# Kernel tuning notes

Measured on AMD Instinct MI355X. Metric: run time of the kernel, lower is better.

The kernel has to match this reference:

```python
import jax, jax.numpy as jnp
import numpy as np

B, N, D, H = 4, 1024, 1024, 16
DH = D // H
MLP = 4 * D
EPS = 1e-6


def setup_inputs() -> dict:
    key = jax.random.key(0)
    ks = jax.random.split(key, 16)
    s = lambda fan_in: 1.0 / np.sqrt(fan_in)
    inp = {
        "x": jax.random.normal(ks[0], (B, N, D), jnp.float32),
        "c": jax.random.normal(ks[1], (B, D), jnp.float32),
        # weights stored (in, out); torch Linear is x @ W.T + b
        "Wq": jax.random.normal(ks[2], (D, D), jnp.float32) * s(D),
        "bq": jnp.zeros((D,), jnp.float32),
        "Wkv": jax.random.normal(ks[3], (D, 2 * D), jnp.float32) * s(D),
        "bkv": jnp.zeros((2 * D,), jnp.float32),
        "Wo": jax.random.normal(ks[4], (D, D), jnp.float32) * s(D),
        "bo": jnp.zeros((D,), jnp.float32),
        "W1": jax.random.normal(ks[5], (D, MLP), jnp.float32) * s(D),
        "b1": jnp.zeros((MLP,), jnp.float32),
        "W2": jax.random.normal(ks[6], (MLP, D), jnp.float32) * s(MLP),
        "b2": jnp.zeros((D,), jnp.float32),
        "Wada": jax.random.normal(ks[7], (D, 6 * D), jnp.float32) * s(D),
        "bada": jnp.zeros((6 * D,), jnp.float32),
    }
    return inp


def _layernorm(h):
    mu = jnp.mean(h, axis=-1, keepdims=True)
    var = jnp.mean(jnp.square(h - mu), axis=-1, keepdims=True)
    return (h - mu) / jnp.sqrt(var + EPS)


def _modulate(h, shift, scale):
    return h * (1.0 + scale[:, None, :]) + shift[:, None, :]


def reference(x, c, Wq, bq, Wkv, bkv, Wo, bo, W1, b1, W2, b2, Wada, bada):
    scale = DH ** -0.5
    mod = jax.nn.silu(c) @ Wada + bada  # [B, 6D]
    sh_msa, sc_msa, g_msa, sh_mlp, sc_mlp, g_mlp = jnp.split(mod, 6, axis=-1)

    # --- attention branch ---
    h = _modulate(_layernorm(x), sh_msa, sc_msa)
    q = (h @ Wq + bq).reshape(B, N, H, DH)
    kv = h @ Wkv + bkv
    k, v = jnp.split(kv, 2, axis=-1)
    k = k.reshape(B, N, H, DH)
    v = v.reshape(B, N, H, DH)
    sim = jnp.einsum("bihd,bjhd->bhij", q, k) * scale  # [B,H,N,N]
    attn = jax.nn.softmax(sim, axis=-1)
    out = jnp.einsum("bhij,bjhd->bihd", attn, v).reshape(B, N, D)
    out = out @ Wo + bo
    x = x + g_msa[:, None, :] * out

    # --- MLP branch ---
    h2 = _modulate(_layernorm(x), sh_mlp, sc_mlp)
    m = jax.nn.gelu(h2 @ W1 + b1, approximate=True) @ W2 + b2
    x = x + g_mlp[:, None, :] * m
    return x
```

## Files before the change

kernel.cpp:

```cpp
#include <hip/hip_runtime.h>
#include <hip/hip_bf16.h>
#include <cstdint>

typedef __attribute__((ext_vector_type(4))) float f32x4;
typedef __attribute__((ext_vector_type(16))) float f32x16;
typedef __attribute__((ext_vector_type(8))) short s16x8;
typedef __attribute__((ext_vector_type(4))) unsigned u32x4;
typedef unsigned short u16;

#define B_  4
#define N_  1024
#define D_  1024
#define H_  16
#define DH_ 64
#define M_  4096
#define SIXD 6144

#define WAITV(n) asm volatile("s_waitcnt vmcnt(" #n ")" ::: "memory")

__device__ __forceinline__ u16 f2bf(float f) {
    unsigned u = __builtin_bit_cast(unsigned, f);
    unsigned r = (u + 0x7fffu + ((u >> 16) & 1u)) >> 16;
    return (u16)r;
}

__device__ __forceinline__ unsigned cvtpk(float a, float b) {
    unsigned r;
    asm("v_cvt_pk_bf16_f32 %0, %1, %2" : "=v"(r) : "v"(a), "v"(b));
    return r;
}

__device__ __forceinline__ void gload16(const void* g, void* l) {
    __builtin_amdgcn_global_load_lds((const __attribute__((address_space(1))) void*)g,
                                     (__attribute__((address_space(3))) void*)l,
                                     16, 0, 0);
}

__global__ __launch_bounds__(256) void prep_all(const float* __restrict__ Wq,
                                                const float* __restrict__ Wkv,
                                                const float* __restrict__ Wo,
                                                const float* __restrict__ W1,
                                                const float* __restrict__ W2,
                                                const float* __restrict__ c,
                                                const float* __restrict__ Wada,
                                                u16* __restrict__ wqkvT,
                                                u16* __restrict__ woT,
                                                u16* __restrict__ w1T,
                                                u16* __restrict__ w2T,
                                                float* __restrict__ modp) {
    int id = blockIdx.x;
    int tid = threadIdx.x;
    if (id < 768) {
        __shared__ float sc[128];
        int colblk = id % 24, b = (id / 24) & 3, ks = id / 96;
        int col = colblk * 256 + tid;
        int k0 = ks * 128;
        if (tid < 128) {
            float v = c[b * D_ + k0 + tid];
            sc[tid] = v / (1.f + __expf(-v));
        }
        __syncthreads();
        float a0 = 0.f, a1 = 0.f, a2 = 0.f, a3 = 0.f;
#pragma unroll 4
        for (int k = 0; k < 128; k += 4) {
            a0 = fmaf(sc[k + 0], Wada[(size_t)(k0 + k + 0) * SIXD + col], a0);
            a1 = fmaf(sc[k + 1], Wada[(size_t)(k0 + k + 1) * SIXD + col], a1);
            a2 = fmaf(sc[k + 2], Wada[(size_t)(k0 + k + 2) * SIXD + col], a2);
            a3 = fmaf(sc[k + 3], Wada[(size_t)(k0 + k + 3) * SIXD + col], a3);
        }
        modp[(size_t)(ks * 4 + b) * SIXD + col] = (a0 + a1) + (a2 + a3);
        return;
    }
    int t_ = id - 768;
    const float* in; u16* outp; int R, C, loc;
    if (t_ < 256)       { in = Wq;  outp = wqkvT;           R = 1024; C = 1024; loc = t_; }
    else if (t_ < 768)  { in = Wkv; outp = wqkvT + 1048576; R = 1024; C = 2048; loc = t_ - 256; }
    else if (t_ < 1024) { in = Wo;  outp = woT;             R = 1024; C = 1024; loc = t_ - 768; }
    else if (t_ < 2048) { in = W1;  outp = w1T;             R = 1024; C = 4096; loc = t_ - 1024; }
    else                { in = W2;  outp = w2T;             R = 4096; C = 1024; loc = t_ - 2048; }
    int tpc = C >> 6;
    int bx = loc % tpc, by = loc / tpc;
    __shared__ float t[64][65];
    int r0 = by * 64, c0 = bx * 64;
    int l16 = tid & 15, grp = tid >> 4;
#pragma unroll
    for (int i = 0; i < 4; ++i) {
        int rr = grp + 16 * i;
        float4 v = *(const float4*)(in + (size_t)(r0 + rr) * C + c0 + l16 * 4);
        t[rr][l16 * 4 + 0] = v.x;
        t[rr][l16 * 4 + 1] = v.y;
        t[rr][l16 * 4 + 2] = v.z;
        t[rr][l16 * 4 + 3] = v.w;
    }
    __syncthreads();
#pragma unroll
    for (int i = 0; i < 4; ++i) {
        int cc = grp + 16 * i;
        ushort4 o;
        o.x = f2bf(t[l16 * 4 + 0][cc]);
        o.y = f2bf(t[l16 * 4 + 1][cc]);
        o.z = f2bf(t[l16 * 4 + 2][cc]);
        o.w = f2bf(t[l16 * 4 + 3][cc]);
        *(ushort4*)(outp + (size_t)(c0 + cc) * R + r0 + l16 * 4) = o;
    }
}

__global__ __launch_bounds__(256) void reduce_mod(const float* __restrict__ modp,
                                                  const float* __restrict__ bada,
                                                  float* __restrict__ mod) {
    int col = blockIdx.x * 256 + threadIdx.x;
    int b = blockIdx.y;
    float s = bada[col];
#pragma unroll
    for (int ks = 0; ks < 8; ++ks)
        s += modp[(size_t)(ks * 4 + b) * SIXD + col];
    mod[b * SIXD + col] = s;
}

__global__ __launch_bounds__(256) void ln_mod(const float* __restrict__ x,
                                              const float* __restrict__ mod,
                                              int shift_c, int scale_c,
                                              u16* __restrict__ h) {
    int row = blockIdx.x;
    int b = row >> 10;
    int tid = threadIdx.x, w = tid >> 6;
    float4 xv = ((const float4*)(x + (size_t)row * D_))[tid];
    float s  = xv.x + xv.y + xv.z + xv.w;
    float s2 = xv.x * xv.x + xv.y * xv.y + xv.z * xv.z + xv.w * xv.w;
#pragma unroll
    for (int m = 1; m <= 32; m <<= 1) { s += __shfl_xor(s, m); s2 += __shfl_xor(s2, m); }
    __shared__ float red[8];
    if ((tid & 63) == 0) { red[w * 2] = s; red[w * 2 + 1] = s2; }
    __syncthreads();
    float S  = red[0] + red[2] + red[4] + red[6];
    float S2 = red[1] + red[3] + red[5] + red[7];
    float mu = S * (1.f / D_);
    float var = S2 * (1.f / D_) - mu * mu;
    float rstd = rsqrtf(var + 1e-6f);
    int d0 = tid * 4;
    float4 shv = *(const float4*)(mod + b * SIXD + shift_c * D_ + d0);
    float4 scv = *(const float4*)(mod + b * SIXD + scale_c * D_ + d0);
    ushort4 o;
    o.x = f2bf((xv.x - mu) * rstd * (1.f + scv.x) + shv.x);
    o.y = f2bf((xv.y - mu) * rstd * (1.f + scv.y) + shv.y);
    o.z = f2bf((xv.z - mu) * rstd * (1.f + scv.z) + shv.z);
    o.w = f2bf((xv.w - mu) * rstd * (1.f + scv.w) + shv.w);
    *(ushort4*)(h + (size_t)row * D_ + d0) = o;
}

__global__ __launch_bounds__(512) void gemm_qkv(const u16* __restrict__ A,
                                                const u16* __restrict__ Bt,
                                                const float* __restrict__ bias,
                                                const float* __restrict__ bias2,
                                                u16* __restrict__ out,
                                                int M, int Nn, int K) {
    __shared__ char lds[2][32768];
    const int tid = threadIdx.x;
    const int w = tid >> 6, lane = tid & 63;
    const int li = lane & 15, lg = lane >> 4;
    const int nwg = gridDim.x * gridDim.y;
    const int flat = blockIdx.y * gridDim.x + blockIdx.x;
    const int wg = (flat & 7) * (nwg >> 3) + (flat >> 3);
    const int m0 = (wg / gridDim.x) * 128, n0 = (wg % gridDim.x) * 128;
    const int wr = w >> 1, wc = w & 1;

    f32x4 acc[2][4];
#pragma unroll
    for (int i = 0; i < 2; ++i)
#pragma unroll
        for (int j = 0; j < 4; ++j) acc[i][j] = (f32x4){0.f, 0.f, 0.f, 0.f};

    auto STAGE = [&](int kk, char* buf) {
#pragma unroll
        for (int j = 0; j < 4; ++j) {
            int basec = j * 512 + w * 64;
            int idx = basec + lane;
            int idl = idx & 1023;
            int row = idl >> 3, cc = idl & 7;
            const u16* src;
            if (idx < 1024)
                src = A + (size_t)(m0 + row) * K + kk + ((cc ^ (row & 7)) << 3);
            else
                src = Bt + (size_t)(n0 + row) * K + kk + ((cc ^ (row & 7)) << 3);
            gload16(src, buf + basec * 16);
        }
    };

    const int nt = K >> 6;
    STAGE(0, lds[0]);
    __syncthreads();
    int cur = 0;
    for (int t = 0; t < nt; ++t) {
        if (t + 1 < nt) { STAGE((t + 1) << 6, lds[cur ^ 1]); WAITV(4); }
        else WAITV(0);
        __builtin_amdgcn_s_barrier();
        __builtin_amdgcn_sched_barrier(0);
        const char* Ab = lds[cur];
        const char* Bb = lds[cur] + 16384;
#pragma unroll
        for (int hh = 0; hh < 2; ++hh) {
            s16x8 af[2], bfr[4];
#pragma unroll
            for (int mi = 0; mi < 2; ++mi) {
                int r = wr * 32 + mi * 16 + li;
                af[mi] = *(const s16x8*)(Ab + r * 128 + (((hh * 4 + lg) ^ (r & 7)) << 4));
            }
#pragma unroll
            for (int nj = 0; nj < 4; ++nj) {
                int r = wc * 64 + nj * 16 + li;
                bfr[nj] = *(const s16x8*)(Bb + r * 128 + (((hh * 4 + lg) ^ (r & 7)) << 4));
            }
#pragma unroll
            for (int mi = 0; mi < 2; ++mi)
#pragma unroll
                for (int nj = 0; nj < 4; ++nj)
                    acc[mi][nj] = __builtin_amdgcn_mfma_f32_16x16x32_bf16(
                        af[mi], bfr[nj], acc[mi][nj], 0, 0, 0);
        }
        __builtin_amdgcn_s_barrier();
        cur ^= 1;
    }

#pragma unroll
    for (int mi = 0; mi < 2; ++mi) {
#pragma unroll
        for (int nj = 0; nj < 4; ++nj) {
            int col = n0 + wc * 64 + nj * 16 + li;
            float bv = (col < D_) ? bias[col] : bias2[col - D_];
#pragma unroll
            for (int rg = 0; rg < 4; ++rg) {
                int grow = m0 + wr * 32 + mi * 16 + 4 * lg + rg;
                float v = acc[mi][nj][rg] + bv;
                int b = grow >> 10, n = grow & 1023;
                if (col < D_) {
                    int hd = col >> 6, dh = col & 63;
                    out[(((size_t)(b * H_ + hd)) * N_ + n) * DH_ + dh] = f2bf(v);
                } else if (col < 2 * D_) {
                    int c2 = col - D_;
                    int hd = c2 >> 6, dh = c2 & 63;
                    out[4194304u + (((size_t)(b * H_ + hd)) * N_ + n) * DH_ + dh] = f2bf(v);
                } else {
                    int c2 = col - 2 * D_;
                    int hd = c2 >> 6, dh = c2 & 63;
                    out[8388608u + (((size_t)(b * H_ + hd)) * DH_ + dh) * N_ + n] = f2bf(v);
                }
            }
        }
    }
}

template <int EPI>
__global__ __launch_bounds__(512) void gemm_bt(const u16* __restrict__ A,
                                               const u16* __restrict__ Bt,
                                               const float* __restrict__ bias,
                                               void* __restrict__ out,
                                               const float* __restrict__ xres,
                                               const float* __restrict__ mod,
                                               int M, int Nn, int K, int gate_c) {
    __shared__ char lds[2][32768];
    const int tid = threadIdx.x;
    const int w = tid >> 6, lane = tid & 63;
    const int li = lane & 15, lg = lane >> 4;
    const int nwg = gridDim.x * gridDim.y;
    const int flat = blockIdx.y * gridDim.x + blockIdx.x;
    const int wg = (flat & 7) * (nwg >> 3) + (flat >> 3);
    const int m0 = (wg / gridDim.x) * 128, n0 = (wg % gridDim.x) * 128;
    const int wr = w >> 1, wc = w & 1;

    f32x4 acc[2][4];
#pragma unroll
    for (int i = 0; i < 2; ++i)
#pragma unroll
        for (int j = 0; j < 4; ++j) acc[i][j] = (f32x4){0.f, 0.f, 0.f, 0.f};

    auto STAGE = [&](int kk, char* buf) {
#pragma unroll
        for (int j = 0; j < 4; ++j) {
            int basec = j * 512 + w * 64;
            int idx = basec + lane;
            int idl = idx & 1023;
            int row = idl >> 3, cc = idl & 7;
            const u16* src;
            if (idx < 1024)
                src = A + (size_t)(m0 + row) * K + kk + ((cc ^ (row & 7)) << 3);
            else
                src = Bt + (size_t)(n0 + row) * K + kk + ((cc ^ (row & 7)) << 3);
            gload16(src, buf + basec * 16);
        }
    };

    const int nt = K >> 6;
    STAGE(0, lds[0]);
    __syncthreads();
    int cur = 0;
    for (int t = 0; t < nt; ++t) {
        if (t + 1 < nt) { STAGE((t + 1) << 6, lds[cur ^ 1]); WAITV(4); }
        else WAITV(0);
        __builtin_amdgcn_s_barrier();
        __builtin_amdgcn_sched_barrier(0);
        const char* Ab = lds[cur];
        const char* Bb = lds[cur] + 16384;
#pragma unroll
        for (int hh = 0; hh < 2; ++hh) {
            s16x8 af[2], bfr[4];
#pragma unroll
            for (int mi = 0; mi < 2; ++mi) {
                int r = wr * 32 + mi * 16 + li;
                af[mi] = *(const s16x8*)(Ab + r * 128 + (((hh * 4 + lg) ^ (r & 7)) << 4));
            }
#pragma unroll
            for (int nj = 0; nj < 4; ++nj) {
                int r = wc * 64 + nj * 16 + li;
                bfr[nj] = *(const s16x8*)(Bb + r * 128 + (((hh * 4 + lg) ^ (r & 7)) << 4));
            }
#pragma unroll
            for (int mi = 0; mi < 2; ++mi)
#pragma unroll
                for (int nj = 0; nj < 4; ++nj)
                    acc[mi][nj] = __builtin_amdgcn_mfma_f32_16x16x32_bf16(
                        af[mi], bfr[nj], acc[mi][nj], 0, 0, 0);
        }
        __builtin_amdgcn_s_barrier();
        cur ^= 1;
    }

#pragma unroll
    for (int mi = 0; mi < 2; ++mi) {
#pragma unroll
        for (int nj = 0; nj < 4; ++nj) {
            int col = n0 + wc * 64 + nj * 16 + li;
            float bv = bias[col];
#pragma unroll
            for (int rg = 0; rg < 4; ++rg) {
                int grow = m0 + wr * 32 + mi * 16 + 4 * lg + rg;
                float v = acc[mi][nj][rg] + bv;
                int b = grow >> 10;
                size_t off = (size_t)grow * D_ + col;
                float g = mod[b * SIXD + gate_c * D_ + col];
                ((float*)out)[off] = xres[off] + g * v;
            }
        }
    }
}

__global__ __launch_bounds__(512, 2) void gemm256_gelu(const u16* __restrict__ A,
                                                       const u16* __restrict__ Bt,
                                                       const float* __restrict__ bias,
                                                       u16* __restrict__ out,
                                                       int M, int Nn, int K) {
    __shared__ char lds[2][65536];
    const int tid = threadIdx.x;
    const int w = tid >> 6, lane = tid & 63;
    const int li = lane & 15, lg = lane >> 4;
    const int wr = w >> 1, wc = w & 1;

    const int flat = blockIdx.x;
    const int wg = (flat & 7) * 32 + (flat >> 3);
    const int mg = wg >> 6, r_ = wg & 63;
    const int mt = mg * 4 + (r_ & 3), nt_ = r_ >> 2;
    const int m0 = mt * 256, n0 = nt_ * 256;

    f32x4 acc[4][8];
#pragma unroll
    for (int i = 0; i < 4; ++i)
#pragma unroll
        for (int j = 0; j < 8; ++j) acc[i][j] = (f32x4){0.f, 0.f, 0.f, 0.f};

    auto STAGE = [&](int kk, char* buf) {
#pragma unroll
        for (int j = 0; j < 4; ++j) {
            int basec = j * 512 + w * 64;
            int idx = basec + lane;
            int row = idx >> 3, cc = idx & 7;
            gload16(A + (size_t)(m0 + row) * K + kk + ((cc ^ (row & 7)) << 3),
                    buf + basec * 16);
            gload16(Bt + (size_t)(n0 + row) * K + kk + ((cc ^ (row & 7)) << 3),
                    buf + 32768 + basec * 16);
        }
    };

    const int nt = K >> 6;
    STAGE(0, lds[0]);
    __syncthreads();
    int cur = 0;
    for (int t = 0; t < nt; ++t) {
        if (t + 1 < nt) STAGE((t + 1) << 6, lds[cur ^ 1]);
        const char* Ab = lds[cur];
        const char* Bb = lds[cur] + 32768;
#pragma unroll
        for (int hh = 0; hh < 2; ++hh) {
            s16x8 af[4], bfr[8];
#pragma unroll
            for (int mi = 0; mi < 4; ++mi) {
                int r = wr * 64 + mi * 16 + li;
                af[mi] = *(const s16x8*)(Ab + r * 128 + (((hh * 4 + lg) ^ (r & 7)) << 4));
            }
#pragma unroll
            for (int nj = 0; nj < 8; ++nj) {
                int r = wc * 128 + nj * 16 + li;
                bfr[nj] = *(const s16x8*)(Bb + r * 128 + (((hh * 4 + lg) ^ (r & 7)) << 4));
            }
#pragma unroll
            for (int mi = 0; mi < 4; ++mi)
#pragma unroll
                for (int nj = 0; nj < 8; ++nj)
                    acc[mi][nj] = __builtin_amdgcn_mfma_f32_16x16x32_bf16(
                        af[mi], bfr[nj], acc[mi][nj], 0, 0, 0);
        }
        __syncthreads();
        cur ^= 1;
    }

#pragma unroll
    for (int nj = 0; nj < 8; ++nj) {
        int col = n0 + wc * 128 + nj * 16 + li;
        float bv = bias[col];
#pragma unroll
        for (int mi = 0; mi < 4; ++mi) {
#pragma unroll
            for (int rg = 0; rg < 4; ++rg) {
                int grow = m0 + wr * 64 + mi * 16 + 4 * lg + rg;
                float v = acc[mi][nj][rg] + bv;
                float u = 0.7978845608028654f * v * (1.f + 0.044715f * v * v);
                u = fminf(fmaxf(u, -15.f), 15.f);
                float e = __expf(2.f * u);
                float th = (e - 1.f) / (e + 1.f);
                out[(size_t)grow * (size_t)Nn + col] = f2bf(0.5f * v * (1.f + th));
            }
        }
    }
}

__global__ __launch_bounds__(256) void attn2(const u16* __restrict__ q,
                                             const u16* __restrict__ k,
                                             const u16* __restrict__ vt,
                                             u16* __restrict__ o) {
    __shared__ __align__(16) char qs[16384];
    __shared__ __align__(16) char kv[2][16384];
    const int tid = threadIdx.x, w = tid >> 6, lane = tid & 63;
    const int l31 = lane & 31, hi = lane >> 5;
    const int flat = blockIdx.x;
    const int wgs = (flat & 7) * 64 + (flat >> 3);
    const int bh = wgs >> 3, qt = wgs & 7;
    const size_t base = (size_t)bh * (N_ * DH_);
    const int q0 = qt * 128;

#pragma unroll
    for (int j = 0; j < 4; ++j) {
        int basec = j * 256 + w * 64;
        int idx = basec + lane;
        int row = idx >> 3, cc = idx & 7;
        gload16(q + base + (size_t)(q0 + row) * DH_ + ((cc ^ (row & 7)) << 3),
                qs + basec * 16);
    }
    auto STAGEKV = [&](int t, char* buf) {
#pragma unroll
        for (int j = 0; j < 4; ++j) {
            int basec = j * 256 + w * 64;
            int idx = basec + lane;
            if (idx < 512) {
                int row = idx >> 3, cc = idx & 7;
                gload16(k + base + (size_t)(t * 64 + row) * DH_ + ((cc ^ (row & 7)) << 3),
                        buf + basec * 16);
            } else {
                int i2 = idx - 512;
                int row = i2 >> 3, cc = i2 & 7;
                gload16(vt + base + (size_t)row * N_ + t * 64 + ((cc ^ (row & 7)) << 3),
                        buf + basec * 16);
            }
        }
    };
    STAGEKV(0, kv[0]);
    __syncthreads();

    s16x8 qf[4];
    const int qr = w * 32 + l31;
#pragma unroll
    for (int st = 0; st < 4; ++st)
        qf[st] = *(const s16x8*)(qs + qr * 128 + (((st * 2 + hi) ^ (qr & 7)) << 4));

    f32x16 oa[2];
#pragma unroll
    for (int r = 0; r < 16; ++r) { oa[0][r] = 0.f; oa[1][r] = 0.f; }
    float mrow = -3e38f, lrow = 0.f;
    const float CSC = 0.125f * 1.44269504088896f;

    int cur = 0;
    for (int t = 0; t < 16; ++t) {
        if (t + 1 < 16) STAGEKV(t + 1, kv[cur ^ 1]);
        const char* Kb = kv[cur];
        const char* Vb = kv[cur] + 8192;

        f32x16 s[2];
#pragma unroll
        for (int r = 0; r < 16; ++r) { s[0][r] = 0.f; s[1][r] = 0.f; }
#pragma unroll
        for (int st = 0; st < 4; ++st) {
#pragma unroll
            for (int ks = 0; ks < 2; ++ks) {
                int r = ks * 32 + l31;
                s16x8 ka = *(const s16x8*)(Kb + r * 128 + (((st * 2 + hi) ^ (r & 7)) << 4));
                s[ks] = __builtin_amdgcn_mfma_f32_32x32x16_bf16(ka, qf[st], s[ks], 0, 0, 0);
            }
        }

        float tmax = s[0][0];
#pragma unroll
        for (int r = 1; r < 16; ++r) tmax = fmaxf(tmax, s[0][r]);
#pragma unroll
        for (int r = 0; r < 16; ++r) tmax = fmaxf(tmax, s[1][r]);
        tmax = fmaxf(tmax, __shfl_xor(tmax, 32));
        float mn = fmaxf(mrow, tmax);
        float al = __builtin_amdgcn_exp2f((mrow - mn) * CSC);
        float nmc = -mn * CSC;
        float rs0 = 0.f, rs1 = 0.f;
#pragma unroll
        for (int r = 0; r < 16; ++r) {
            float p0 = __builtin_amdgcn_exp2f(fmaf(s[0][r], CSC, nmc));
            float p1 = __builtin_amdgcn_exp2f(fmaf(s[1][r], CSC, nmc));
            s[0][r] = p0; s[1][r] = p1;
            rs0 += p0; rs1 += p1;
        }
        float rs = rs0 + rs1;
        rs += __shfl_xor(rs, 32);
        lrow = lrow * al + rs;
        mrow = mn;
#pragma unroll
        for (int r = 0; r < 16; ++r) { oa[0][r] *= al; oa[1][r] *= al; }

        unsigned u[16];
#pragma unroll
        for (int ks = 0; ks < 2; ++ks)
#pragma unroll
            for (int j = 0; j < 4; ++j) {
                u[ks * 8 + 2 * j]     = cvtpk(s[ks][4 * j + 0], s[ks][4 * j + 1]);
                u[ks * 8 + 2 * j + 1] = cvtpk(s[ks][4 * j + 2], s[ks][4 * j + 3]);
            }

#pragma unroll
        for (int kstep = 0; kstep < 4; ++kstep) {
            unsigned b0 = u[kstep * 4 + 0], b1 = u[kstep * 4 + 1];
            unsigned b2 = u[kstep * 4 + 2], b3 = u[kstep * 4 + 3];
            asm volatile("v_permlane32_swap_b32 %0, %1" : "+v"(b0), "+v"(b2));
            asm volatile("v_permlane32_swap_b32 %0, %1" : "+v"(b1), "+v"(b3));
            u32x4 pbu = (u32x4){b0, b1, b2, b3};
            s16x8 pb = __builtin_bit_cast(s16x8, pbu);
#pragma unroll
            for (int ds = 0; ds < 2; ++ds) {
                int r = ds * 32 + l31;
                s16x8 va = *(const s16x8*)(Vb + r * 128 + (((kstep * 2 + hi) ^ (r & 7)) << 4));
                oa[ds] = __builtin_amdgcn_mfma_f32_32x32x16_bf16(va, pb, oa[ds], 0, 0, 0);
            }
        }
        __syncthreads();
        cur ^= 1;
    }

    float inv = 1.f / lrow;
#pragma unroll
    for (int ds = 0; ds < 2; ++ds)
#pragma unroll
        for (int j = 0; j < 4; ++j)
#pragma unroll
            for (int t2 = 0; t2 < 2; ++t2) {
                unsigned pk = cvtpk(oa[ds][4 * j + 2 * t2] * inv,
                                    oa[ds][4 * j + 2 * t2 + 1] * inv);
                int row = qr;
                int dch = 4 * ds + j;
                *(unsigned*)(qs + row * 128 + ((dch ^ (row & 7)) << 4) +
                             (4 * hi + 2 * t2) * 2) = pk;
            }
    __syncthreads();
    {
        int r = tid >> 1, h2 = tid & 1;
        const int b = bh >> 4, hd = bh & 15;
        size_t obase = ((size_t)(b * N_ + q0 + r)) * D_ + hd * DH_;
#pragma unroll
        for (int c = 0; c < 4; ++c) {
            int c2 = h2 * 4 + c;
            s16x8 v = *(const s16x8*)(qs + r * 128 + ((c2 ^ (r & 7)) << 4));
            *(s16x8*)(o + obase + c2 * 8) = v;
        }
    }
}

extern "C" void kernel_launch(void* const* d_in, const int* in_sizes, int n_in,
                              void* d_out, int out_size, void* d_ws, size_t ws_size,
                              hipStream_t stream) {
    const float* x    = (const float*)d_in[0];
    const float* c    = (const float*)d_in[1];
    const float* Wq   = (const float*)d_in[2];
    const float* bq   = (const float*)d_in[3];
    const float* Wkv  = (const float*)d_in[4];
    const float* bkv  = (const float*)d_in[5];
    const float* Wo   = (const float*)d_in[6];
    const float* bo   = (const float*)d_in[7];
    const float* W1   = (const float*)d_in[8];
    const float* b1   = (const float*)d_in[9];
    const float* W2   = (const float*)d_in[10];
    const float* b2   = (const float*)d_in[11];
    const float* Wada = (const float*)d_in[12];
    const float* bada = (const float*)d_in[13];

    char* ws = (char*)d_ws;
    const size_t MB = 1024 * 1024;
    u16*   wqkvT = (u16*)(ws + 0);
    u16*   woT  = (u16*)(ws + 6 * MB);
    u16*   w1T  = (u16*)(ws + 8 * MB);
    u16*   w2T  = (u16*)(ws + 16 * MB);
    float* mod  = (float*)(ws + 24 * MB);
    float* modp = (float*)(ws + 24 * MB + 131072);
    u16*   h    = (u16*)(ws + 25 * MB);
    u16*   qb   = (u16*)(ws + 33 * MB);
    u16*   ao   = (u16*)(ws + 57 * MB);
    float* x1   = (float*)(ws + 65 * MB);
    u16*   m1   = (u16*)(ws + 33 * MB);
    float* outp = (float*)d_out;

    prep_all<<<3840, 256, 0, stream>>>(Wq, Wkv, Wo, W1, W2, c, Wada,
                                       wqkvT, woT, w1T, w2T, modp);
    reduce_mod<<<dim3(24, 4), 256, 0, stream>>>(modp, bada, mod);

    ln_mod<<<M_, 256, 0, stream>>>(x, mod, 0, 1, h);

    gemm_qkv<<<dim3(24, 32), 512, 0, stream>>>(h, wqkvT, bq, bkv, qb, M_, 3 * D_, D_);

    attn2<<<512, 256, 0, stream>>>(qb, qb + 4194304, qb + 8388608, ao);

    gemm_bt<2><<<dim3(8, 32), 512, 0, stream>>>(ao, woT, bo, x1, x, mod, M_, D_, D_, 2);

    ln_mod<<<M_, 256, 0, stream>>>(x1, mod, 3, 4, h);

    gemm256_gelu<<<256, 512, 0, stream>>>(h, w1T, b1, m1, M_, 4 * D_, D_);
    gemm_bt<4><<<dim3(8, 32), 512, 0, stream>>>(m1, w2T, b2, outp, x1, mod, M_, D_, 4 * D_, 5);
}
```

Baseline: 217.2 us.

## Fold modulation reduction into LN and QKV GEMM, raise MFMA priority in attention

Removes the standalone reduce_mod launch. The first LayerNorm now sums the split-K partials of the modulation vector inline. The full mod buffer is reduced by 48 extra blocks appended to the QKV GEMM grid, which is flattened to 1D with a hardcoded swizzle. Separately, s_setprio raises wave priority around the MFMA sections in the attention kernel so matrix work gets issued ahead of other waves. In exchange, every LN block re-reads 8 partials per element, and the GEMM tile mapping is hardcoded to these shapes.

```diff
diff --git a/kernel.cpp b/kernel.cpp
--- a/kernel.cpp
+++ b/kernel.cpp
@@ -105,20 +105,10 @@
     }
 }
 
-__global__ __launch_bounds__(256) void reduce_mod(const float* __restrict__ modp,
-                                                  const float* __restrict__ bada,
-                                                  float* __restrict__ mod) {
-    int col = blockIdx.x * 256 + threadIdx.x;
-    int b = blockIdx.y;
-    float s = bada[col];
-#pragma unroll
-    for (int ks = 0; ks < 8; ++ks)
-        s += modp[(size_t)(ks * 4 + b) * SIXD + col];
-    mod[b * SIXD + col] = s;
-}
-
+template <int INLINE_MOD>
 __global__ __launch_bounds__(256) void ln_mod(const float* __restrict__ x,
-                                              const float* __restrict__ mod,
+                                              const float* __restrict__ msrc,
+                                              const float* __restrict__ bada,
                                               int shift_c, int scale_c,
                                               u16* __restrict__ h) {
     int row = blockIdx.x;
@@ -138,8 +128,22 @@
     float var = S2 * (1.f / D_) - mu * mu;
     float rstd = rsqrtf(var + 1e-6f);
     int d0 = tid * 4;
-    float4 shv = *(const float4*)(mod + b * SIXD + shift_c * D_ + d0);
-    float4 scv = *(const float4*)(mod + b * SIXD + scale_c * D_ + d0);
+    float4 shv, scv;
+    if (INLINE_MOD) {
+        shv = *(const float4*)(bada + shift_c * D_ + d0);
+        scv = *(const float4*)(bada + scale_c * D_ + d0);
+#pragma unroll
+        for (int ks = 0; ks < 8; ++ks) {
+            const float* p = msrc + (size_t)(ks * 4 + b) * SIXD;
+            float4 p1 = *(const float4*)(p + shift_c * D_ + d0);
+            float4 p2 = *(const float4*)(p + scale_c * D_ + d0);
+            shv.x += p1.x; shv.y += p1.y; shv.z += p1.z; shv.w += p1.w;
+            scv.x += p2.x; scv.y += p2.y; scv.z += p2.z; scv.w += p2.w;
+        }
+    } else {
+        shv = *(const float4*)(msrc + b * SIXD + shift_c * D_ + d0);
+        scv = *(const float4*)(msrc + b * SIXD + scale_c * D_ + d0);
+    }
     ushort4 o;
     o.x = f2bf((xv.x - mu) * rstd * (1.f + scv.x) + shv.x);
     o.y = f2bf((xv.y - mu) * rstd * (1.f + scv.y) + shv.y);
@@ -153,15 +157,27 @@
                                                 const float* __restrict__ bias,
                                                 const float* __restrict__ bias2,
                                                 u16* __restrict__ out,
+                                                const float* __restrict__ modp,
+                                                const float* __restrict__ bada,
+                                                float* __restrict__ mod,
                                                 int M, int Nn, int K) {
+    if (blockIdx.x >= 768) {
+        int idx = (blockIdx.x - 768) * 512 + threadIdx.x;
+        int b = idx / SIXD, col = idx % SIXD;
+        float s = bada[col];
+#pragma unroll
+        for (int ks = 0; ks < 8; ++ks)
+            s += modp[(size_t)(ks * 4 + b) * SIXD + col];
+        mod[b * SIXD + col] = s;
+        return;
+    }
     __shared__ char lds[2][32768];
     const int tid = threadIdx.x;
     const int w = tid >> 6, lane = tid & 63;
     const int li = lane & 15, lg = lane >> 4;
-    const int nwg = gridDim.x * gridDim.y;
-    const int flat = blockIdx.y * gridDim.x + blockIdx.x;
-    const int wg = (flat & 7) * (nwg >> 3) + (flat >> 3);
-    const int m0 = (wg / gridDim.x) * 128, n0 = (wg % gridDim.x) * 128;
+    const int flat = blockIdx.x;
+    const int wg = (flat & 7) * 96 + (flat >> 3);
+    const int m0 = (wg / 24) * 128, n0 = (wg % 24) * 128;
     const int wr = w >> 1, wc = w & 1;
 
     f32x4 acc[2][4];
@@ -494,6 +510,7 @@
         f32x16 s[2];
 #pragma unroll
         for (int r = 0; r < 16; ++r) { s[0][r] = 0.f; s[1][r] = 0.f; }
+        __builtin_amdgcn_s_setprio(1);
 #pragma unroll
         for (int st = 0; st < 4; ++st) {
 #pragma unroll
@@ -503,6 +520,7 @@
                 s[ks] = __builtin_amdgcn_mfma_f32_32x32x16_bf16(ka, qf[st], s[ks], 0, 0, 0);
             }
         }
+        __builtin_amdgcn_s_setprio(0);
 
         float tmax = s[0][0];
 #pragma unroll
@@ -545,12 +563,14 @@
             asm volatile("v_permlane32_swap_b32 %0, %1" : "+v"(b1), "+v"(b3));
             u32x4 pbu = (u32x4){b0, b1, b2, b3};
             s16x8 pb = __builtin_bit_cast(s16x8, pbu);
+            __builtin_amdgcn_s_setprio(1);
 #pragma unroll
             for (int ds = 0; ds < 2; ++ds) {
                 int r = ds * 32 + l31;
                 s16x8 va = *(const s16x8*)(Vb + r * 128 + (((kstep * 2 + hi) ^ (r & 7)) << 4));
                 oa[ds] = __builtin_amdgcn_mfma_f32_32x32x16_bf16(va, pb, oa[ds], 0, 0, 0);
             }
+            __builtin_amdgcn_s_setprio(0);
         }
         __syncthreads();
         cur ^= 1;
@@ -619,17 +639,17 @@
 
     prep_all<<<3840, 256, 0, stream>>>(Wq, Wkv, Wo, W1, W2, c, Wada,
                                        wqkvT, woT, w1T, w2T, modp);
-    reduce_mod<<<dim3(24, 4), 256, 0, stream>>>(modp, bada, mod);
-
-    ln_mod<<<M_, 256, 0, stream>>>(x, mod, 0, 1, h);
-
-    gemm_qkv<<<dim3(24, 32), 512, 0, stream>>>(h, wqkvT, bq, bkv, qb, M_, 3 * D_, D_);
+
+    ln_mod<1><<<M_, 256, 0, stream>>>(x, modp, bada, 0, 1, h);
+
+    gemm_qkv<<<816, 512, 0, stream>>>(h, wqkvT, bq, bkv, qb, modp, bada, mod,
+                                      M_, 3 * D_, D_);
 
     attn2<<<512, 256, 0, stream>>>(qb, qb + 4194304, qb + 8388608, ao);
 
     gemm_bt<2><<<dim3(8, 32), 512, 0, stream>>>(ao, woT, bo, x1, x, mod, M_, D_, D_, 2);
 
-    ln_mod<<<M_, 256, 0, stream>>>(x1, mod, 3, 4, h);
+    ln_mod<0><<<M_, 256, 0, stream>>>(x1, mod, bada, 3, 4, h);
 
     gemm256_gelu<<<256, 512, 0, stream>>>(h, w1T, b1, m1, M_, 4 * D_, D_);
     gemm_bt<4><<<dim3(8, 32), 512, 0, stream>>>(m1, w2T, b2, outp, x1, mod, M_, D_, 4 * D_, 5);
```

After: 224.3 us. +3.3%, slower.
